# Performance work log

Hardware: AMD Instinct MI355X
Metric: run time of the kernel (lower is better)

The kernel has to match this reference:

```python
import jax, jax.numpy as jnp
import numpy as np

B, S, E = 8, 2048, 512
VOCAB, FVOCAB = 32000, 128
SCALE = float(np.power(E, 0.5))  # emb_size ** (0.5 * temper), temper=1


def setup_inputs() -> dict:
    key = jax.random.key(0)
    ks = jax.random.split(key, 7)
    key_seq = jax.random.randint(ks[0], (B, S), 0, VOCAB, dtype=jnp.int32)
    value_seq = jax.random.randint(ks[1], (B, S), 0, FVOCAB, dtype=jnp.int32)
    hidden = jax.random.normal(ks[2], (B, S, E), dtype=jnp.float32)
    mask_matrix = jax.random.uniform(ks[3], (B, S, S), dtype=jnp.float32)
    nan_matrix = jnp.zeros((1,), dtype=jnp.int32)  # unused by forward
    # learned params; padding_idx=0 -> zero row in embeddings
    key_emb = jax.random.normal(ks[4], (VOCAB, E), dtype=jnp.float32).at[0].set(0.0)
    value_emb = jax.random.normal(ks[5], (FVOCAB, E), dtype=jnp.float32).at[0].set(0.0)
    weight = jax.random.normal(ks[6], (E, E), dtype=jnp.float32) / np.sqrt(E)
    return {
        "key_seq": key_seq, "value_seq": value_seq, "hidden": hidden,
        "mask_matrix": mask_matrix, "nan_matrix": nan_matrix,
        "key_emb": key_emb, "value_emb": value_emb, "weight": weight,
    }


def reference(key_seq, value_seq, hidden, mask_matrix, nan_matrix,
              key_emb, value_emb, weight):
    k = key_emb[key_seq]          # [B,S,E]
    v = value_emb[value_seq]      # [B,S,E]
    q = jnp.einsum('bsd,de->bse', hidden, weight)   # hidden @ weight
    u = jnp.einsum('bse,bte->bst', q, k) / SCALE    # QK^T, [B,S,S]
    mask = jnp.clip(mask_matrix.astype(u.dtype), 0.0, 1.0)
    exp_u = jnp.exp(u)
    delta = exp_u * mask
    p = delta / (jnp.sum(delta, axis=2, keepdims=True) + 1e-10)
    o = jnp.einsum('bst,bte->bse', p, v)            # PV, [B,S,E]
    return o
```

## Files before the change

### kernel.cpp

```cpp
#include <hip/hip_runtime.h>
#include <stdint.h>

#define BB 8
#define SS 2048
#define EE 512
#define INV_SCALE 0.04419417382415922f

typedef __attribute__((ext_vector_type(8))) short bf8_t;
typedef __attribute__((ext_vector_type(4))) float f4_t;

__device__ __forceinline__ unsigned short f2bf(float f) {
    union { float f; uint32_t u; } x; x.f = f;
    uint32_t r = x.u + 0x7fffu + ((x.u >> 16) & 1u);
    return (unsigned short)(r >> 16);
}


__global__ void __launch_bounds__(256) gather_k_kernel(const int* __restrict__ idx,
                                                       const float* __restrict__ emb,
                                                       unsigned short* __restrict__ out) {
    int id = blockIdx.x * 256 + threadIdx.x;
    int chunk = id & 63;
    int row = id >> 6;
    int e0 = chunk * 8;
    int k = idx[row];
    const float* src = emb + (size_t)k * EE + e0;
    float4 a = *(const float4*)(src);
    float4 c = *(const float4*)(src + 4);
    union { unsigned short s[8]; int4 v; } u;
    u.s[0] = f2bf(a.x); u.s[1] = f2bf(a.y); u.s[2] = f2bf(a.z); u.s[3] = f2bf(a.w);
    u.s[4] = f2bf(c.x); u.s[5] = f2bf(c.y); u.s[6] = f2bf(c.z); u.s[7] = f2bf(c.w);
    *(int4*)(out + (size_t)row * EE + e0) = u.v;
}

__global__ void __launch_bounds__(256) cast_h_kernel(const float* __restrict__ in,
                                                     unsigned short* __restrict__ out) {
    int id = blockIdx.x * 256 + threadIdx.x;
    const float* src = in + (size_t)id * 8;
    float4 a = *(const float4*)(src);
    float4 c = *(const float4*)(src + 4);
    union { unsigned short s[8]; int4 v; } u;
    u.s[0] = f2bf(a.x); u.s[1] = f2bf(a.y); u.s[2] = f2bf(a.z); u.s[3] = f2bf(a.w);
    u.s[4] = f2bf(c.x); u.s[5] = f2bf(c.y); u.s[6] = f2bf(c.z); u.s[7] = f2bf(c.w);
    *(int4*)(out + (size_t)id * 8) = u.v;
}

__global__ void __launch_bounds__(256) gather_vt_kernel(const int* __restrict__ idx,
                                                        const float* __restrict__ emb,
                                                        unsigned short* __restrict__ vt) {
    int id = blockIdx.x * 256 + threadIdx.x;
    int t = id & (SS - 1);
    int rest = id >> 11;
    int e = rest & (EE - 1);
    int b = rest >> 9;
    int k = idx[b * SS + t];
    vt[id] = f2bf(emb[(size_t)k * EE + e]);
}

__global__ void __launch_bounds__(256) transpose_w_kernel(const float* __restrict__ w,
                                                          unsigned short* __restrict__ wt) {
    int id = blockIdx.x * 256 + threadIdx.x;
    int e = id & (EE - 1);
    int f = id >> 9;
    wt[id] = f2bf(w[(size_t)e * EE + f] * INV_SCALE);
}


__device__ __forceinline__ void stage_tile(const unsigned short* gbase, int ld, int k0,
                                           unsigned short* lds, int wave, int lane) {
    const int srcchunk = ((lane & 3) ^ ((lane >> 3) & 3)) * 8;
#pragma unroll
    for (int i = 0; i < 2; ++i) {
        int row = i * 64 + wave * 16 + (lane >> 2);
        const unsigned short* g = gbase + (size_t)row * ld + k0 + srcchunk;
        unsigned short* l = lds + i * 2048 + wave * 512 + lane * 8;
        __builtin_amdgcn_global_load_lds((const __attribute__((address_space(1))) unsigned int*)g,
                                         (__attribute__((address_space(3))) unsigned int*)l,
                                         16, 0, 0);
    }
}

template <int KLEN>
__device__ __forceinline__ void mfma_loop(const unsigned short* Abase, int lda,
                                          const unsigned short* Bbase, int ldb,
                                          unsigned short* As, unsigned short* Bs,
                                          f4_t acc[4][4], int wave, int lane) {
    const int wm = wave >> 1, wn = wave & 1, quad = lane >> 4, l16 = lane & 15;
    const int qs = (quad ^ ((l16 >> 1) & 3)) * 8;
    constexpr int NT = KLEN / 32;

    stage_tile(Abase, lda, 0, As, wave, lane);
    stage_tile(Bbase, ldb, 0, Bs, wave, lane);
    __syncthreads();

    int cur = 0;
#pragma unroll 1
    for (int t = 0; t < NT; ++t) {
        if (t + 1 < NT) {
            stage_tile(Abase, lda, (t + 1) * 32, As + ((cur ^ 1) << 12), wave, lane);
            stage_tile(Bbase, ldb, (t + 1) * 32, Bs + ((cur ^ 1) << 12), wave, lane);
        }
        const unsigned short* a = As + (cur << 12);
        const unsigned short* b = Bs + (cur << 12);
        bf8_t af[4], bfr[4];
#pragma unroll
        for (int mi = 0; mi < 4; ++mi)
            af[mi] = *(const bf8_t*)(a + (wm * 64 + mi * 16 + l16) * 32 + qs);
#pragma unroll
        for (int ni = 0; ni < 4; ++ni)
            bfr[ni] = *(const bf8_t*)(b + (wn * 64 + ni * 16 + l16) * 32 + qs);
#pragma unroll
        for (int mi = 0; mi < 4; ++mi)
#pragma unroll
            for (int ni = 0; ni < 4; ++ni)
                acc[mi][ni] = __builtin_amdgcn_mfma_f32_16x16x32_bf16(af[mi], bfr[ni],
                                                                      acc[mi][ni], 0, 0, 0);
        __syncthreads();
        cur ^= 1;
    }
}


__global__ void __launch_bounds__(256) qgen_kernel(const unsigned short* __restrict__ H,
                                                   const unsigned short* __restrict__ Wt,
                                                   unsigned short* __restrict__ Q) {
    __shared__ unsigned short As[2 * 128 * 32];
    __shared__ unsigned short Bs[2 * 128 * 32];
    const int tid = threadIdx.x, wave = tid >> 6, lane = tid & 63;
    const int rowT = blockIdx.y;
    const int colT = blockIdx.x;
    f4_t acc[4][4];
    const f4_t z = {0.f, 0.f, 0.f, 0.f};
    for (int i = 0; i < 4; ++i) for (int j = 0; j < 4; ++j) acc[i][j] = z;
    mfma_loop<EE>(H + (size_t)rowT * 128 * EE, EE,
                  Wt + (size_t)colT * 128 * EE, EE, As, Bs, acc, wave, lane);
    const int wm = wave >> 1, wn = wave & 1, quad = lane >> 4, l16 = lane & 15;
#pragma unroll
    for (int mi = 0; mi < 4; ++mi)
#pragma unroll
        for (int r = 0; r < 4; ++r) {
            int row = rowT * 128 + wm * 64 + mi * 16 + quad * 4 + r;
#pragma unroll
            for (int ni = 0; ni < 4; ++ni) {
                int col = colT * 128 + wn * 64 + ni * 16 + l16;
                Q[(size_t)row * EE + col] = f2bf(acc[mi][ni][r]);
            }
        }
}

__global__ void __launch_bounds__(256) qk_kernel(const unsigned short* __restrict__ Q,
                                                 const unsigned short* __restrict__ K,
                                                 const float* __restrict__ mask,
                                                 unsigned short* __restrict__ delta,
                                                 float* __restrict__ lsum) {
    __shared__ unsigned short As[2 * 128 * 32];
    __shared__ unsigned short Bs[2 * 128 * 32];
    const int tid = threadIdx.x, wave = tid >> 6, lane = tid & 63;
    const int b = blockIdx.z, qT = blockIdx.y, tT = blockIdx.x;
    f4_t acc[4][4];
    const f4_t z = {0.f, 0.f, 0.f, 0.f};
    for (int i = 0; i < 4; ++i) for (int j = 0; j < 4; ++j) acc[i][j] = z;
    mfma_loop<EE>(Q + ((size_t)b * SS + qT * 128) * EE, EE,
                  K + ((size_t)b * SS + tT * 128) * EE, EE, As, Bs, acc, wave, lane);
    const int wm = wave >> 1, wn = wave & 1, quad = lane >> 4, l16 = lane & 15;
#pragma unroll
    for (int mi = 0; mi < 4; ++mi)
#pragma unroll
        for (int r = 0; r < 4; ++r) {
            int row = qT * 128 + wm * 64 + mi * 16 + quad * 4 + r;
            const float* mrow = mask + ((size_t)b * SS + row) * SS;
            unsigned short* drow = delta + ((size_t)b * SS + row) * SS;
            float psum = 0.f;
#pragma unroll
            for (int ni = 0; ni < 4; ++ni) {
                int col = tT * 128 + wn * 64 + ni * 16 + l16;
                float m = mrow[col];
                m = fminf(fmaxf(m, 0.f), 1.f);
                float e = __expf(acc[mi][ni][r]) * m;
                drow[col] = f2bf(e);
                psum += e;
            }
#pragma unroll
            for (int off = 1; off < 16; off <<= 1)
                psum += __shfl_xor(psum, off, 16);
            if (l16 == 0) atomicAdd(&lsum[b * SS + row], psum);
        }
}

__global__ void __launch_bounds__(256) pv_kernel(const unsigned short* __restrict__ delta,
                                                 const unsigned short* __restrict__ Vt,
                                                 const float* __restrict__ lsum,
                                                 float* __restrict__ out) {
    __shared__ unsigned short As[2 * 128 * 32];
    __shared__ unsigned short Bs[2 * 128 * 32];
    const int tid = threadIdx.x, wave = tid >> 6, lane = tid & 63;
    const int b = blockIdx.z, qT = blockIdx.y, eT = blockIdx.x;
    f4_t acc[4][4];
    const f4_t z = {0.f, 0.f, 0.f, 0.f};
    for (int i = 0; i < 4; ++i) for (int j = 0; j < 4; ++j) acc[i][j] = z;
    mfma_loop<SS>(delta + ((size_t)b * SS + qT * 128) * SS, SS,
                  Vt + ((size_t)b * EE + eT * 128) * SS, SS, As, Bs, acc, wave, lane);
    const int wm = wave >> 1, wn = wave & 1, quad = lane >> 4, l16 = lane & 15;
#pragma unroll
    for (int mi = 0; mi < 4; ++mi)
#pragma unroll
        for (int r = 0; r < 4; ++r) {
            int row = qT * 128 + wm * 64 + mi * 16 + quad * 4 + r;
            float inv = 1.0f / (lsum[b * SS + row] + 1e-10f);
#pragma unroll
            for (int ni = 0; ni < 4; ++ni) {
                int col = eT * 128 + wn * 64 + ni * 16 + l16;
                out[((size_t)b * SS + row) * EE + col] = acc[mi][ni][r] * inv;
            }
        }
}


extern "C" void kernel_launch(void* const* d_in, const int* in_sizes, int n_in,
                              void* d_out, int out_size, void* d_ws, size_t ws_size,
                              hipStream_t stream) {
    const int*   key_seq = (const int*)d_in[0];
    const int*   val_seq = (const int*)d_in[1];
    const float* hidden  = (const float*)d_in[2];
    const float* mask    = (const float*)d_in[3];
    const float* key_emb = (const float*)d_in[5];
    const float* val_emb = (const float*)d_in[6];
    const float* weight  = (const float*)d_in[7];
    float* out = (float*)d_out;

    char* ws = (char*)d_ws;
    const size_t SZ_BSE = (size_t)BB * SS * EE * sizeof(unsigned short);
    unsigned short* Q    = (unsigned short*)(ws);
    unsigned short* K    = (unsigned short*)(ws + SZ_BSE);
    unsigned short* Vt   = (unsigned short*)(ws + 2 * SZ_BSE);
    unsigned short* H    = (unsigned short*)(ws + 3 * SZ_BSE);
    unsigned short* Wt   = (unsigned short*)(ws + 4 * SZ_BSE);
    float*          lsum = (float*)(ws + 4 * SZ_BSE + 524288);
    unsigned short* delta= (unsigned short*)(ws + 4 * SZ_BSE + 524288 + 65536);

    hipMemsetAsync(lsum, 0, (size_t)BB * SS * sizeof(float), stream);

    gather_k_kernel<<<4096, 256, 0, stream>>>(key_seq, key_emb, K);
    cast_h_kernel<<<4096, 256, 0, stream>>>(hidden, H);
    gather_vt_kernel<<<32768, 256, 0, stream>>>(val_seq, val_emb, Vt);
    transpose_w_kernel<<<1024, 256, 0, stream>>>(weight, Wt);

    qgen_kernel<<<dim3(4, 128), 256, 0, stream>>>(H, Wt, Q);
    qk_kernel<<<dim3(16, 16, 8), 256, 0, stream>>>(Q, K, mask, delta, lsum);
    pv_kernel<<<dim3(4, 16, 8), 256, 0, stream>>>(delta, Vt, lsum, out);
}
```

Measured before the change: 436.4 us.

## Fuse QK, masked exp, and PV into one flash-style attention kernel

Replaces the separate QK kernel, which wrote the bf16 delta matrix and atomically accumulated row sums, and the PV kernel with one fused kernel. Each block owns 64 query rows of one batch and loops over key tiles, staging the exp*mask probabilities in LDS and accumulating PV in registers. This removes the large delta write and reread and the global lsum memset. In exchange only 256 blocks of 512 threads run, so parallelism is lower. V fragments are read straight from global memory without LDS staging, and Q is reloaded for every key tile.

```diff
diff --git a/kernel.cpp b/kernel.cpp
--- a/kernel.cpp
+++ b/kernel.cpp
@@ -72,7 +72,7 @@
 #pragma unroll
     for (int i = 0; i < 2; ++i) {
         int row = i * 64 + wave * 16 + (lane >> 2);
-        const unsigned short* g = gbase + (size_t)row * ld + k0 + srcchunk;
+        const unsigned short* g = gbase + (size_t)row * ld + (k0 + srcchunk);
         unsigned short* l = lds + i * 2048 + wave * 512 + lane * 8;
         __builtin_amdgcn_global_load_lds((const __attribute__((address_space(1))) unsigned int*)g,
                                          (__attribute__((address_space(3))) unsigned int*)l,
@@ -119,7 +119,6 @@
         cur ^= 1;
     }
 }
-
 
 __global__ void __launch_bounds__(256) qgen_kernel(const unsigned short* __restrict__ H,
                                                    const unsigned short* __restrict__ Wt,
@@ -148,70 +147,175 @@
         }
 }
 
-__global__ void __launch_bounds__(256) qk_kernel(const unsigned short* __restrict__ Q,
-                                                 const unsigned short* __restrict__ K,
-                                                 const float* __restrict__ mask,
-                                                 unsigned short* __restrict__ delta,
-                                                 float* __restrict__ lsum) {
-    __shared__ unsigned short As[2 * 128 * 32];
-    __shared__ unsigned short Bs[2 * 128 * 32];
-    const int tid = threadIdx.x, wave = tid >> 6, lane = tid & 63;
-    const int b = blockIdx.z, qT = blockIdx.y, tT = blockIdx.x;
-    f4_t acc[4][4];
+__global__ void __launch_bounds__(512, 2) attn_fused_kernel(
+    const unsigned short* __restrict__ Q,
+    const unsigned short* __restrict__ K,
+    const unsigned short* __restrict__ Vt,
+    const float* __restrict__ mask,
+    float* __restrict__ out) {
+    __shared__ unsigned short As[2][64 * 64];
+    __shared__ unsigned short Bs[2][128 * 64];
+    __shared__ unsigned short Pl[64 * 128];
+    __shared__ float lsum_s[64];
+
+    const int tid = threadIdx.x;
+    const int wave = tid >> 6, lane = tid & 63;
+    const int wm = wave >> 2, wn = wave & 3;
+    const int quad = lane >> 4, l16 = lane & 15;
+
+    const int bid = blockIdx.x;
+    const int b = bid & 7, qT = bid >> 3;
+
+    const unsigned short* Qbase = Q + ((size_t)b * SS + qT * 64) * EE;
+    const unsigned short* Kbase = K + (size_t)b * SS * EE;
+    const unsigned short* Vbase = Vt + (size_t)b * EE * SS;
+    const float* mbase = mask + ((size_t)b * SS + qT * 64) * SS;
+
+    if (tid < 64) lsum_s[tid] = 0.f;
+
+    f4_t pvacc[2][8];
     const f4_t z = {0.f, 0.f, 0.f, 0.f};
-    for (int i = 0; i < 4; ++i) for (int j = 0; j < 4; ++j) acc[i][j] = z;
-    mfma_loop<EE>(Q + ((size_t)b * SS + qT * 128) * EE, EE,
-                  K + ((size_t)b * SS + tT * 128) * EE, EE, As, Bs, acc, wave, lane);
-    const int wm = wave >> 1, wn = wave & 1, quad = lane >> 4, l16 = lane & 15;
-#pragma unroll
-    for (int mi = 0; mi < 4; ++mi)
+#pragma unroll
+    for (int i = 0; i < 2; ++i)
+#pragma unroll
+        for (int j = 0; j < 8; ++j) pvacc[i][j] = z;
+    float psum[2][4] = {{0.f, 0.f, 0.f, 0.f}, {0.f, 0.f, 0.f, 0.f}};
+
+    const int srow = tid >> 3;
+    const int scA = ((tid & 7) ^ (srow & 7)) * 8;
+
+#pragma unroll 1
+    for (int tT = 0; tT < 16; ++tT) {
+        const unsigned short* Kt = Kbase + (size_t)tT * 128 * EE;
+
+        f4_t sacc[2][2];
+#pragma unroll
+        for (int i = 0; i < 2; ++i)
+#pragma unroll
+            for (int j = 0; j < 2; ++j) sacc[i][j] = z;
+
+        {
+            const unsigned short* gA = Qbase + (size_t)srow * EE + scA;
+            __builtin_amdgcn_global_load_lds(
+                (const __attribute__((address_space(1))) unsigned int*)gA,
+                (__attribute__((address_space(3))) unsigned int*)(&As[0][0] + tid * 8),
+                16, 0, 0);
+#pragma unroll
+            for (int i = 0; i < 2; ++i) {
+                const unsigned short* gB = Kt + (size_t)(i * 64 + srow) * EE + scA;
+                __builtin_amdgcn_global_load_lds(
+                    (const __attribute__((address_space(1))) unsigned int*)gB,
+                    (__attribute__((address_space(3))) unsigned int*)(&Bs[0][0] + i * 4096 + tid * 8),
+                    16, 0, 0);
+            }
+        }
+        __syncthreads();
+
+        int buf = 0;
+#pragma unroll 1
+        for (int s = 0; s < 8; ++s) {
+            if (s + 1 < 8) {
+                const int k0 = (s + 1) * 64;
+                const unsigned short* gA = Qbase + (size_t)srow * EE + k0 + scA;
+                __builtin_amdgcn_global_load_lds(
+                    (const __attribute__((address_space(1))) unsigned int*)gA,
+                    (__attribute__((address_space(3))) unsigned int*)(&As[buf ^ 1][0] + tid * 8),
+                    16, 0, 0);
+#pragma unroll
+                for (int i = 0; i < 2; ++i) {
+                    const unsigned short* gB = Kt + (size_t)(i * 64 + srow) * EE + k0 + scA;
+                    __builtin_amdgcn_global_load_lds(
+                        (const __attribute__((address_space(1))) unsigned int*)gB,
+                        (__attribute__((address_space(3))) unsigned int*)(&Bs[buf ^ 1][0] + i * 4096 + tid * 8),
+                        16, 0, 0);
+                }
+            }
+            bf8_t af[2][2], bfv[2][2];
+#pragma unroll
+            for (int mi = 0; mi < 2; ++mi)
+#pragma unroll
+                for (int ks = 0; ks < 2; ++ks)
+                    af[mi][ks] = *(const bf8_t*)(&As[buf][0] +
+                        (wm * 32 + mi * 16 + l16) * 64 + (((ks * 4 + quad) ^ (l16 & 7)) << 3));
+#pragma unroll
+            for (int ni = 0; ni < 2; ++ni)
+#pragma unroll
+                for (int ks = 0; ks < 2; ++ks)
+                    bfv[ni][ks] = *(const bf8_t*)(&Bs[buf][0] +
+                        (wn * 32 + ni * 16 + l16) * 64 + (((ks * 4 + quad) ^ (l16 & 7)) << 3));
+#pragma unroll
+            for (int ks = 0; ks < 2; ++ks)
+#pragma unroll
+                for (int mi = 0; mi < 2; ++mi)
+#pragma unroll
+                    for (int ni = 0; ni < 2; ++ni)
+                        sacc[mi][ni] = __builtin_amdgcn_mfma_f32_16x16x32_bf16(
+                            af[mi][ks], bfv[ni][ks], sacc[mi][ni], 0, 0, 0);
+            __syncthreads();
+            buf ^= 1;
+        }
+
+#pragma unroll
+        for (int mi = 0; mi < 2; ++mi)
+#pragma unroll
+            for (int ni = 0; ni < 2; ++ni)
+#pragma unroll
+                for (int r = 0; r < 4; ++r) {
+                    const int row_l = wm * 32 + mi * 16 + quad * 4 + r;
+                    const int t_l = wn * 32 + ni * 16 + l16;
+                    float m = mbase[(size_t)row_l * SS + tT * 128 + t_l];
+                    m = fminf(fmaxf(m, 0.f), 1.f);
+                    float e = __expf(sacc[mi][ni][r]) * m;
+                    psum[mi][r] += e;
+                    const int c = t_l >> 3;
+                    Pl[row_l * 128 + ((c ^ (row_l & 7)) << 3) + (t_l & 7)] = f2bf(e);
+                }
+        __syncthreads();
+
+#pragma unroll
+        for (int ks = 0; ks < 4; ++ks) {
+            bf8_t pa[2];
+#pragma unroll
+            for (int mi = 0; mi < 2; ++mi)
+                pa[mi] = *(const bf8_t*)(&Pl[0] +
+                    (wm * 32 + mi * 16 + l16) * 128 + (((ks * 4 + quad) ^ (l16 & 7)) << 3));
+            bf8_t bv[8];
+#pragma unroll
+            for (int ni = 0; ni < 8; ++ni)
+                bv[ni] = *(const bf8_t*)(Vbase +
+                    (size_t)(wn * 128 + ni * 16 + l16) * SS + tT * 128 + ks * 32 + quad * 8);
+#pragma unroll
+            for (int mi = 0; mi < 2; ++mi)
+#pragma unroll
+                for (int ni = 0; ni < 8; ++ni)
+                    pvacc[mi][ni] = __builtin_amdgcn_mfma_f32_16x16x32_bf16(
+                        pa[mi], bv[ni], pvacc[mi][ni], 0, 0, 0);
+        }
+        __syncthreads();
+    }
+
+#pragma unroll
+    for (int mi = 0; mi < 2; ++mi)
 #pragma unroll
         for (int r = 0; r < 4; ++r) {
-            int row = qT * 128 + wm * 64 + mi * 16 + quad * 4 + r;
-            const float* mrow = mask + ((size_t)b * SS + row) * SS;
-            unsigned short* drow = delta + ((size_t)b * SS + row) * SS;
-            float psum = 0.f;
-#pragma unroll
-            for (int ni = 0; ni < 4; ++ni) {
-                int col = tT * 128 + wn * 64 + ni * 16 + l16;
-                float m = mrow[col];
-                m = fminf(fmaxf(m, 0.f), 1.f);
-                float e = __expf(acc[mi][ni][r]) * m;
-                drow[col] = f2bf(e);
-                psum += e;
-            }
+            float p = psum[mi][r];
 #pragma unroll
             for (int off = 1; off < 16; off <<= 1)
-                psum += __shfl_xor(psum, off, 16);
-            if (l16 == 0) atomicAdd(&lsum[b * SS + row], psum);
-        }
-}
-
-__global__ void __launch_bounds__(256) pv_kernel(const unsigned short* __restrict__ delta,
-                                                 const unsigned short* __restrict__ Vt,
-                                                 const float* __restrict__ lsum,
-                                                 float* __restrict__ out) {
-    __shared__ unsigned short As[2 * 128 * 32];
-    __shared__ unsigned short Bs[2 * 128 * 32];
-    const int tid = threadIdx.x, wave = tid >> 6, lane = tid & 63;
-    const int b = blockIdx.z, qT = blockIdx.y, eT = blockIdx.x;
-    f4_t acc[4][4];
-    const f4_t z = {0.f, 0.f, 0.f, 0.f};
-    for (int i = 0; i < 4; ++i) for (int j = 0; j < 4; ++j) acc[i][j] = z;
-    mfma_loop<SS>(delta + ((size_t)b * SS + qT * 128) * SS, SS,
-                  Vt + ((size_t)b * EE + eT * 128) * SS, SS, As, Bs, acc, wave, lane);
-    const int wm = wave >> 1, wn = wave & 1, quad = lane >> 4, l16 = lane & 15;
-#pragma unroll
-    for (int mi = 0; mi < 4; ++mi)
+                p += __shfl_xor(p, off, 16);
+            if (l16 == 0)
+                atomicAdd(&lsum_s[wm * 32 + mi * 16 + quad * 4 + r], p);
+        }
+    __syncthreads();
+#pragma unroll
+    for (int mi = 0; mi < 2; ++mi)
 #pragma unroll
         for (int r = 0; r < 4; ++r) {
-            int row = qT * 128 + wm * 64 + mi * 16 + quad * 4 + r;
-            float inv = 1.0f / (lsum[b * SS + row] + 1e-10f);
-#pragma unroll
-            for (int ni = 0; ni < 4; ++ni) {
-                int col = eT * 128 + wn * 64 + ni * 16 + l16;
-                out[((size_t)b * SS + row) * EE + col] = acc[mi][ni][r] * inv;
-            }
+            const int row_l = wm * 32 + mi * 16 + quad * 4 + r;
+            const float inv = 1.0f / (lsum_s[row_l] + 1e-10f);
+            const size_t orow = ((size_t)b * SS + qT * 64 + row_l) * EE;
+#pragma unroll
+            for (int ni = 0; ni < 8; ++ni)
+                out[orow + wn * 128 + ni * 16 + l16] = pvacc[mi][ni][r] * inv;
         }
 }
 
@@ -230,15 +334,11 @@
 
     char* ws = (char*)d_ws;
     const size_t SZ_BSE = (size_t)BB * SS * EE * sizeof(unsigned short);
-    unsigned short* Q    = (unsigned short*)(ws);
-    unsigned short* K    = (unsigned short*)(ws + SZ_BSE);
-    unsigned short* Vt   = (unsigned short*)(ws + 2 * SZ_BSE);
-    unsigned short* H    = (unsigned short*)(ws + 3 * SZ_BSE);
-    unsigned short* Wt   = (unsigned short*)(ws + 4 * SZ_BSE);
-    float*          lsum = (float*)(ws + 4 * SZ_BSE + 524288);
-    unsigned short* delta= (unsigned short*)(ws + 4 * SZ_BSE + 524288 + 65536);
-
-    hipMemsetAsync(lsum, 0, (size_t)BB * SS * sizeof(float), stream);
+    unsigned short* Q  = (unsigned short*)(ws);
+    unsigned short* K  = (unsigned short*)(ws + SZ_BSE);
+    unsigned short* Vt = (unsigned short*)(ws + 2 * SZ_BSE);
+    unsigned short* H  = (unsigned short*)(ws + 3 * SZ_BSE);
+    unsigned short* Wt = (unsigned short*)(ws + 4 * SZ_BSE);
 
     gather_k_kernel<<<4096, 256, 0, stream>>>(key_seq, key_emb, K);
     cast_h_kernel<<<4096, 256, 0, stream>>>(hidden, H);
@@ -246,6 +346,5 @@
     transpose_w_kernel<<<1024, 256, 0, stream>>>(weight, Wt);
 
     qgen_kernel<<<dim3(4, 128), 256, 0, stream>>>(H, Wt, Q);
-    qk_kernel<<<dim3(16, 16, 8), 256, 0, stream>>>(Q, K, mask, delta, lsum);
-    pv_kernel<<<dim3(4, 16, 8), 256, 0, stream>>>(delta, Vt, lsum, out);
-}
+    attn_fused_kernel<<<256, 512, 0, stream>>>(Q, K, Vt, mask, out);
+}
```

After: 504.1 us. 1.16x slower.

## Replace QK kernel with 256x256-tile 8-wave pipelined MFMA kernel

Applied to the files above, without the earlier changes.

Replaces the 128x128-tile QK^T kernel with a 512-thread kernel that computes 256x256 output tiles. It streams K-dimension half-tiles into LDS through a multi-buffered ping-pong schedule with explicit vmcnt waits, barriers and setprio around MFMA bursts. The goal is to raise arithmetic intensity per LDS load and overlap global-to-LDS copies with MFMA work. The cost is many more accumulator registers, 64KB of LDS per block, and a fragile hand-written wait-count schedule.

```diff
diff --git a/kernel.cpp b/kernel.cpp
--- a/kernel.cpp
+++ b/kernel.cpp
@@ -72,7 +72,7 @@
 #pragma unroll
     for (int i = 0; i < 2; ++i) {
         int row = i * 64 + wave * 16 + (lane >> 2);
-        const unsigned short* g = gbase + (size_t)row * ld + k0 + srcchunk;
+        const unsigned short* g = gbase + (size_t)row * ld + (k0 + srcchunk);
         unsigned short* l = lds + i * 2048 + wave * 512 + lane * 8;
         __builtin_amdgcn_global_load_lds((const __attribute__((address_space(1))) unsigned int*)g,
                                          (__attribute__((address_space(3))) unsigned int*)l,
@@ -119,7 +119,6 @@
         cur ^= 1;
     }
 }
-
 
 __global__ void __launch_bounds__(256) qgen_kernel(const unsigned short* __restrict__ H,
                                                    const unsigned short* __restrict__ Wt,
@@ -148,45 +147,6 @@
         }
 }
 
-__global__ void __launch_bounds__(256) qk_kernel(const unsigned short* __restrict__ Q,
-                                                 const unsigned short* __restrict__ K,
-                                                 const float* __restrict__ mask,
-                                                 unsigned short* __restrict__ delta,
-                                                 float* __restrict__ lsum) {
-    __shared__ unsigned short As[2 * 128 * 32];
-    __shared__ unsigned short Bs[2 * 128 * 32];
-    const int tid = threadIdx.x, wave = tid >> 6, lane = tid & 63;
-    const int b = blockIdx.z, qT = blockIdx.y, tT = blockIdx.x;
-    f4_t acc[4][4];
-    const f4_t z = {0.f, 0.f, 0.f, 0.f};
-    for (int i = 0; i < 4; ++i) for (int j = 0; j < 4; ++j) acc[i][j] = z;
-    mfma_loop<EE>(Q + ((size_t)b * SS + qT * 128) * EE, EE,
-                  K + ((size_t)b * SS + tT * 128) * EE, EE, As, Bs, acc, wave, lane);
-    const int wm = wave >> 1, wn = wave & 1, quad = lane >> 4, l16 = lane & 15;
-#pragma unroll
-    for (int mi = 0; mi < 4; ++mi)
-#pragma unroll
-        for (int r = 0; r < 4; ++r) {
-            int row = qT * 128 + wm * 64 + mi * 16 + quad * 4 + r;
-            const float* mrow = mask + ((size_t)b * SS + row) * SS;
-            unsigned short* drow = delta + ((size_t)b * SS + row) * SS;
-            float psum = 0.f;
-#pragma unroll
-            for (int ni = 0; ni < 4; ++ni) {
-                int col = tT * 128 + wn * 64 + ni * 16 + l16;
-                float m = mrow[col];
-                m = fminf(fmaxf(m, 0.f), 1.f);
-                float e = __expf(acc[mi][ni][r]) * m;
-                drow[col] = f2bf(e);
-                psum += e;
-            }
-#pragma unroll
-            for (int off = 1; off < 16; off <<= 1)
-                psum += __shfl_xor(psum, off, 16);
-            if (l16 == 0) atomicAdd(&lsum[b * SS + row], psum);
-        }
-}
-
 __global__ void __launch_bounds__(256) pv_kernel(const unsigned short* __restrict__ delta,
                                                  const unsigned short* __restrict__ Vt,
                                                  const float* __restrict__ lsum,
@@ -216,6 +176,134 @@
 }
 
 
+__device__ __forceinline__ void stage_half(const unsigned short* base, int t, int kh,
+                                           unsigned short* half_, int tid) {
+#pragma unroll
+    for (int j = 0; j < 2; ++j) {
+        int idx = j * 512 + tid;
+        int r = idx >> 2, slot = idx & 3;
+        int c4 = slot ^ ((r >> 1) & 3);
+        const unsigned short* g = base + (size_t)r * EE + t * 64 + kh * 32 + c4 * 8;
+        __builtin_amdgcn_global_load_lds((const __attribute__((address_space(1))) unsigned int*)g,
+                                         (__attribute__((address_space(3))) unsigned int*)(half_ + idx * 8),
+                                         16, 0, 0);
+    }
+}
+
+template <int NH, int WAIT>
+__device__ __forceinline__ void qk8_phase(const unsigned short* Ah, const unsigned short* Bh,
+                                          bf8_t af[8], f4_t acc[8][4],
+                                          const unsigned short* sbase, int st, int skh,
+                                          unsigned short* sdst, bool sen,
+                                          int wm, int wn, int l16, int aslot, int tid,
+                                          bool lastsel) {
+    if (NH == 0) {
+#pragma unroll
+        for (int mi = 0; mi < 8; ++mi)
+            af[mi] = *(const bf8_t*)(Ah + (wm * 128 + mi * 16 + l16) * 32 + aslot);
+    }
+    bf8_t b0 = *(const bf8_t*)(Bh + (wn * 64 + NH * 32 + l16) * 32 + aslot);
+    bf8_t b1 = *(const bf8_t*)(Bh + (wn * 64 + NH * 32 + 16 + l16) * 32 + aslot);
+    if (sen) stage_half(sbase, st, skh, sdst, tid);
+    if (WAIT >= 0) {
+        if (lastsel) asm volatile("s_waitcnt vmcnt(0)" ::: "memory");
+        else         asm volatile("s_waitcnt vmcnt(6)" ::: "memory");
+    }
+    __builtin_amdgcn_s_barrier();
+    asm volatile("s_waitcnt lgkmcnt(0)" ::: "memory");
+    __builtin_amdgcn_sched_barrier(0);
+    __builtin_amdgcn_s_setprio(1);
+#pragma unroll
+    for (int mi = 0; mi < 8; ++mi) {
+        acc[mi][NH * 2]     = __builtin_amdgcn_mfma_f32_16x16x32_bf16(af[mi], b0, acc[mi][NH * 2], 0, 0, 0);
+        acc[mi][NH * 2 + 1] = __builtin_amdgcn_mfma_f32_16x16x32_bf16(af[mi], b1, acc[mi][NH * 2 + 1], 0, 0, 0);
+    }
+    __builtin_amdgcn_s_setprio(0);
+    __builtin_amdgcn_s_barrier();
+    __builtin_amdgcn_sched_barrier(0);
+}
+
+__global__ void __launch_bounds__(512, 2) qk8_kernel(const unsigned short* __restrict__ Q,
+                                                     const unsigned short* __restrict__ K,
+                                                     const float* __restrict__ mask,
+                                                     unsigned short* __restrict__ delta,
+                                                     float* __restrict__ lsum) {
+    __shared__ unsigned short Ab[2][2][256 * 32];
+    __shared__ unsigned short Bb[2][2][256 * 32];
+    const int tid = threadIdx.x;
+    const int wave = tid >> 6, lane = tid & 63;
+    const int wm = wave >> 2, wn = wave & 3;
+    const int quad = lane >> 4, l16 = lane & 15;
+    const int aslot = (quad ^ ((l16 >> 1) & 3)) * 8;
+
+    const int lin = blockIdx.x;
+    const int b = lin & 7;
+    const int rest = lin >> 3;
+    const int tT = rest & 7, qT = rest >> 3;
+
+    const unsigned short* Abase = Q + ((size_t)b * SS + qT * 256) * EE;
+    const unsigned short* Bbase = K + ((size_t)b * SS + tT * 256) * EE;
+
+    f4_t acc[8][4];
+    const f4_t z = {0.f, 0.f, 0.f, 0.f};
+#pragma unroll
+    for (int i = 0; i < 8; ++i)
+#pragma unroll
+        for (int j = 0; j < 4; ++j) acc[i][j] = z;
+
+    stage_half(Abase, 0, 0, &Ab[0][0][0], tid);
+    stage_half(Bbase, 0, 0, &Bb[0][0][0], tid);
+    stage_half(Abase, 0, 1, &Ab[0][1][0], tid);
+    stage_half(Bbase, 0, 1, &Bb[0][1][0], tid);
+    stage_half(Abase, 1, 0, &Ab[1][0][0], tid);
+    stage_half(Bbase, 1, 0, &Bb[1][0][0], tid);
+    stage_half(Abase, 1, 1, &Ab[1][1][0], tid);
+    asm volatile("s_waitcnt vmcnt(6)" ::: "memory");
+    __builtin_amdgcn_s_barrier();
+    __builtin_amdgcn_sched_barrier(0);
+
+    bf8_t af[8];
+
+#pragma unroll 1
+    for (int it = 0; it < 4; ++it) {
+        const int t1 = 2 * it + 1, t2 = 2 * it + 2, t3 = 2 * it + 3;
+        const bool last = (it == 3);
+        qk8_phase<0, -1>(&Ab[0][0][0], &Bb[0][0][0], af, acc, Bbase, t1, 1, &Bb[1][1][0], true,  wm, wn, l16, aslot, tid, last);
+        qk8_phase<1, -1>(&Ab[0][0][0], &Bb[0][0][0], af, acc, Abase, t2, 0, &Ab[0][0][0], !last, wm, wn, l16, aslot, tid, last);
+        qk8_phase<0, -1>(&Ab[0][1][0], &Bb[0][1][0], af, acc, Bbase, t2, 0, &Bb[0][0][0], !last, wm, wn, l16, aslot, tid, last);
+        qk8_phase<1,  6>(&Ab[0][1][0], &Bb[0][1][0], af, acc, Abase, t2, 1, &Ab[0][1][0], !last, wm, wn, l16, aslot, tid, last);
+        qk8_phase<0, -1>(&Ab[1][0][0], &Bb[1][0][0], af, acc, Bbase, t2, 1, &Bb[0][1][0], !last, wm, wn, l16, aslot, tid, last);
+        qk8_phase<1, -1>(&Ab[1][0][0], &Bb[1][0][0], af, acc, Abase, t3, 0, &Ab[1][0][0], !last, wm, wn, l16, aslot, tid, last);
+        qk8_phase<0, -1>(&Ab[1][1][0], &Bb[1][1][0], af, acc, Bbase, t3, 0, &Bb[1][0][0], !last, wm, wn, l16, aslot, tid, last);
+        qk8_phase<1,  6>(&Ab[1][1][0], &Bb[1][1][0], af, acc, Abase, t3, 1, &Ab[1][1][0], !last, wm, wn, l16, aslot, tid, last);
+    }
+
+#pragma unroll
+    for (int mi = 0; mi < 8; ++mi) {
+#pragma unroll
+        for (int r = 0; r < 4; ++r) {
+            int row = qT * 256 + wm * 128 + mi * 16 + quad * 4 + r;
+            const float* mrow = mask + ((size_t)b * SS + row) * SS;
+            unsigned short* drow = delta + ((size_t)b * SS + row) * SS;
+            float psum = 0.f;
+#pragma unroll
+            for (int j = 0; j < 4; ++j) {
+                int col = tT * 256 + wn * 64 + j * 16 + l16;
+                float m = mrow[col];
+                m = fminf(fmaxf(m, 0.f), 1.f);
+                float e = __expf(acc[mi][j][r]) * m;
+                drow[col] = f2bf(e);
+                psum += e;
+            }
+#pragma unroll
+            for (int off = 1; off < 16; off <<= 1)
+                psum += __shfl_xor(psum, off, 16);
+            if (l16 == 0) atomicAdd(&lsum[b * SS + row], psum);
+        }
+    }
+}
+
+
 extern "C" void kernel_launch(void* const* d_in, const int* in_sizes, int n_in,
                               void* d_out, int out_size, void* d_ws, size_t ws_size,
                               hipStream_t stream) {
@@ -246,6 +334,6 @@
     transpose_w_kernel<<<1024, 256, 0, stream>>>(weight, Wt);
 
     qgen_kernel<<<dim3(4, 128), 256, 0, stream>>>(H, Wt, Q);
-    qk_kernel<<<dim3(16, 16, 8), 256, 0, stream>>>(Q, K, mask, delta, lsum);
+    qk8_kernel<<<512, 512, 0, stream>>>(Q, K, mask, delta, lsum);
     pv_kernel<<<dim3(4, 16, 8), 256, 0, stream>>>(delta, Vt, lsum, out);
 }
```

Result: no change. 428.2 us (-1.9%).
